# Optimization experiments

Measured on AMD Instinct MI355X. Metric: run time of the kernel, lower is better.

## Reference

```python
import jax, jax.numpy as jnp
import numpy as np

B, L, D = 2, 2048, 2048
H, KV, HD = 16, 4, 64  # query heads, kv heads, head_dim
EPS = 1e-6
ROPE_BASE = 10000.0


def setup_inputs() -> dict:
    key = jax.random.key(0)
    k0, k1, k2 = jax.random.split(key, 3)
    x = jax.random.normal(k0, (B, L, D), dtype=jnp.float32)
    W_qkv = jax.random.normal(k1, ((H + 2 * KV) * HD, D), dtype=jnp.float32) * 0.02
    W_out = jax.random.normal(k2, (D, H * HD), dtype=jnp.float32) * 0.02
    q_norm_w = jnp.ones((HD,), dtype=jnp.float32)
    k_norm_w = jnp.ones((HD,), dtype=jnp.float32)
    # causal additive mask (forward's optional `mask` arg)
    mask = jnp.triu(jnp.full((L, L), -1e9, dtype=jnp.float32), k=1)
    return {"x": x, "W_qkv": W_qkv, "W_out": W_out,
            "q_norm_w": q_norm_w, "k_norm_w": k_norm_w, "mask": mask}


def _rms_norm(x, w):
    # normalize over last (head) dim
    var = jnp.mean(x * x, axis=-1, keepdims=True)
    return x * jax.lax.rsqrt(var + EPS) * w


def _rope(x):
    # x: [B, nH, L, HD]; non-traditional (rotate-half) RoPE, offset=0
    half = HD // 2
    freqs = ROPE_BASE ** (-jnp.arange(0, HD, 2, dtype=jnp.float32) / HD)  # [half]
    theta = jnp.arange(L, dtype=jnp.float32)[:, None] * freqs[None, :]    # [L, half]
    cos, sin = jnp.cos(theta), jnp.sin(theta)
    x1, x2 = x[..., :half], x[..., half:]
    return jnp.concatenate([x1 * cos - x2 * sin, x1 * sin + x2 * cos], axis=-1)


def reference(x, W_qkv, W_out, q_norm_w, k_norm_w, mask):
    # fused QKV projection
    qkv = jnp.einsum("bld,ed->ble", x, W_qkv)                       # [B,L,(H+2KV)*HD]
    qkv = qkv.reshape(B, L, H + 2 * KV, HD).transpose(0, 2, 1, 3)   # [B,nH,L,HD]
    q, k, v = jnp.split(qkv, [H, H + KV], axis=1)
    # per-head QK RMSNorm + RoPE
    q = _rope(_rms_norm(q, q_norm_w))
    k = _rope(_rms_norm(k, k_norm_w))
    # GQA: repeat kv heads to match query heads
    rep = H // KV
    k = jnp.repeat(k, rep, axis=1)
    v = jnp.repeat(v, rep, axis=1)
    scale = HD ** -0.5
    scores = jnp.einsum("bhqd,bhkd->bhqk", q, k) * scale + mask      # [B,H,L,L]
    attn = jax.nn.softmax(scores, axis=-1)
    out = jnp.einsum("bhqk,bhkd->bhqd", attn, v)                     # [B,H,L,HD]
    out = out.transpose(0, 2, 1, 3).reshape(B, L, H * HD)
    return jnp.einsum("ble,de->bld", out, W_out)                     # [B,L,D]
```

## Files before the change

### kernel.cpp

```cpp
#include <hip/hip_runtime.h>
#include <hip/hip_bf16.h>


typedef __bf16 bf16;
typedef bf16 bf16x8 __attribute__((ext_vector_type(8)));
typedef bf16 bf16x4 __attribute__((ext_vector_type(4)));
typedef float f32x4 __attribute__((ext_vector_type(4)));

#define L_SEQ 2048
#define NQH 16
#define NKVH 4

__global__ __launch_bounds__(256) void cast_bf16(const float* __restrict__ in,
                                                 bf16* __restrict__ out, int n) {
  int i = (blockIdx.x * 256 + threadIdx.x) * 4;
  if (i < n) {
    float4 v = *(const float4*)&in[i];
    bf16x4 o;
    o[0] = (bf16)v.x; o[1] = (bf16)v.y; o[2] = (bf16)v.z; o[3] = (bf16)v.w;
    *(bf16x4*)&out[i] = o;
  }
}

__global__ __launch_bounds__(256)
void gemm_bt(const bf16* __restrict__ A, const bf16* __restrict__ B,
             float* __restrict__ C, int M, int N, int K) {
  __shared__ bf16 As[128 * 32];
  __shared__ bf16 Bs[128 * 32];
  const int tid = threadIdx.x;
  const int lane = tid & 63, w = tid >> 6;
  const int lq = lane & 15, g = lane >> 4;
  const int wr = w >> 1, wc = w & 1;
  const int bx = blockIdx.x, by = blockIdx.y;

  f32x4 acc[4][4] = {};

  const int nk = K >> 5;
  for (int kt = 0; kt < nk; ++kt) {
#pragma unroll
    for (int c = 0; c < 2; ++c) {
      int idx = c * 256 + tid;
      int row = idx >> 2;
      int ch = idx & 3;
      int pch = ch ^ ((row >> 1) & 3);
      bf16x8 va = *(const bf16x8*)&A[(size_t)(by * 128 + row) * K + kt * 32 + ch * 8];
      *(bf16x8*)&As[row * 32 + pch * 8] = va;
      bf16x8 vb = *(const bf16x8*)&B[(size_t)(bx * 128 + row) * K + kt * 32 + ch * 8];
      *(bf16x8*)&Bs[row * 32 + pch * 8] = vb;
    }
    __syncthreads();
    bf16x8 af[4], bfr[4];
#pragma unroll
    for (int i = 0; i < 4; ++i) {
      int ra = wr * 64 + i * 16 + lq;
      af[i] = *(const bf16x8*)&As[ra * 32 + (g ^ ((ra >> 1) & 3)) * 8];
      int rb = wc * 64 + i * 16 + lq;
      bfr[i] = *(const bf16x8*)&Bs[rb * 32 + (g ^ ((rb >> 1) & 3)) * 8];
    }
#pragma unroll
    for (int i = 0; i < 4; ++i)
#pragma unroll
      for (int j = 0; j < 4; ++j)
        acc[i][j] = __builtin_amdgcn_mfma_f32_16x16x32_bf16(af[i], bfr[j], acc[i][j], 0, 0, 0);
    __syncthreads();
  }
#pragma unroll
  for (int i = 0; i < 4; ++i)
#pragma unroll
    for (int j = 0; j < 4; ++j) {
      int row = by * 128 + wr * 64 + i * 16 + g * 4;
      int col = bx * 128 + wc * 64 + j * 16 + lq;
#pragma unroll
      for (int r = 0; r < 4; ++r) C[(size_t)(row + r) * N + col] = acc[i][j][r];
    }
}

__global__ __launch_bounds__(256)
void norm_rope(const float* __restrict__ qkv, const float* __restrict__ qw,
               const float* __restrict__ kw, bf16* __restrict__ Qb,
               bf16* __restrict__ Kb, bf16* __restrict__ Vb) {
  const int bl = blockIdx.x;
  const int b = bl >> 11, l = bl & (L_SEQ - 1);
  const int w = threadIdx.x >> 6, lane = threadIdx.x & 63;
  const int i = lane & 31;
  float freq = exp2f(-(float)i * 0.41524101186280154f);
  float theta = (float)l * freq;
  float sn, cs;
  sincosf(theta, &sn, &cs);
  float qwl = qw[lane], kwl = kw[lane];

  for (int h = w; h < 24; h += 4) {
    float v = qkv[(size_t)bl * 1536 + h * 64 + lane];
    if (h < 20) {
      float ss = v * v;
#pragma unroll
      for (int off = 32; off; off >>= 1) ss += __shfl_xor(ss, off);
      float rs = rsqrtf(ss * (1.f / 64.f) + 1e-6f);
      float wt = (h < 16) ? qwl : kwl;
      float y = v * rs * wt;
      float part = __shfl_xor(y, 32);
      float out = (lane < 32) ? (y * cs - part * sn) : (part * sn + y * cs);
      if (h < 16)
        Qb[((size_t)(b * NQH + h) * L_SEQ + l) * 64 + lane] = (bf16)(out * 0.125f);
      else
        Kb[((size_t)(b * NKVH + (h - 16)) * L_SEQ + l) * 64 + lane] = (bf16)out;
    } else {
      Vb[((size_t)(b * NKVH + (h - 20)) * L_SEQ + l) * 64 + lane] = (bf16)v;
    }
  }
}

__global__ __launch_bounds__(256)
void transpose_v(const bf16* __restrict__ Vb, bf16* __restrict__ Vt) {
  __shared__ bf16 T[64 * 66];
  const int bk = blockIdx.y;
  const int l0 = blockIdx.x * 64;
  const int t = threadIdx.x;
  const bf16* src = Vb + (size_t)bk * L_SEQ * 64;
#pragma unroll
  for (int c = 0; c < 2; ++c) {
    int idx = c * 256 + t;
    int row = idx >> 3, ch = idx & 7;
    bf16x8 v = *(const bf16x8*)&src[(size_t)(l0 + row) * 64 + ch * 8];
#pragma unroll
    for (int j = 0; j < 8; ++j) T[(ch * 8 + j) * 66 + row] = v[j];
  }
  __syncthreads();
  bf16* dst = Vt + (size_t)bk * 64 * L_SEQ;
#pragma unroll
  for (int c = 0; c < 2; ++c) {
    int idx = c * 256 + t;
    int d = idx >> 3, ch = idx & 7;
    bf16x8 v;
#pragma unroll
    for (int j = 0; j < 8; ++j) v[j] = T[d * 66 + ch * 8 + j];
    *(bf16x8*)&dst[(size_t)d * L_SEQ + l0 + ch * 8] = v;
  }
}

__global__ __launch_bounds__(256)
void attn(const bf16* __restrict__ Qb, const bf16* __restrict__ Kb,
          const bf16* __restrict__ Vt, bf16* __restrict__ Ao) {
  const int qblk = 31 - blockIdx.x;
  const int bh = blockIdx.y;
  const int b = bh >> 4, h = bh & 15, kv = h >> 2;
  const int tid = threadIdx.x;
  const int w = tid >> 6, lane = tid & 63;
  const int lq = lane & 15, g = lane >> 4;

  __shared__ bf16 Ks[64][64];
  __shared__ bf16 Vs[64][64];
  __shared__ bf16 Plds[4][16][72];

  const bf16* Qp = Qb + (size_t)(b * NQH + h) * L_SEQ * 64;
  const bf16* Kp = Kb + (size_t)(b * NKVH + kv) * L_SEQ * 64;
  const bf16* Vp = Vt + (size_t)(b * NKVH + kv) * 64 * L_SEQ;

  const int qr0 = qblk * 64 + w * 16;
  bf16x8 qf[2];
  qf[0] = *(const bf16x8*)&Qp[(qr0 + lq) * 64 + g * 8];
  qf[1] = *(const bf16x8*)&Qp[(qr0 + lq) * 64 + 32 + g * 8];

  const int sr0 = tid >> 3, sc = tid & 7;
  const int sr1 = sr0 + 32;
  const int swc0 = (sc ^ (sr0 & 7)) * 8;
  bf16x8 rk0, rk1, rv0, rv1;

  auto load_tile = [&](int k0) {
    rk0 = *(const bf16x8*)&Kp[(size_t)(k0 + sr0) * 64 + sc * 8];
    rk1 = *(const bf16x8*)&Kp[(size_t)(k0 + sr1) * 64 + sc * 8];
    rv0 = *(const bf16x8*)&Vp[(size_t)sr0 * L_SEQ + k0 + sc * 8];
    rv1 = *(const bf16x8*)&Vp[(size_t)sr1 * L_SEQ + k0 + sc * 8];
  };
  auto write_tile = [&]() {
    *(bf16x8*)&Ks[sr0][swc0] = rk0;
    *(bf16x8*)&Ks[sr1][swc0] = rk1;
    *(bf16x8*)&Vs[sr0][swc0] = rv0;
    *(bf16x8*)&Vs[sr1][swc0] = rv1;
  };

  f32x4 o[4] = {};
  float m = -1e30f, lsum = 0.f;
  const float L2E = 1.4426950408889634f;
  const int qg = qr0 + lq;

  const int nkt = qblk + 1;
  load_tile(0);
  write_tile();
  __syncthreads();

  for (int kt = 0; kt < nkt; ++kt) {
    const int k0 = kt * 64;
    const bool diag = (kt == nkt - 1);
    if (kt + 1 < nkt) load_tile(k0 + 64);

    f32x4 s[4] = {};
#pragma unroll
    for (int ks = 0; ks < 4; ++ks) {
      if (!diag || ks <= w) {
        const int row = ks * 16 + lq, sw = lq & 7;
        bf16x8 kf0 = *(const bf16x8*)&Ks[row][(g ^ sw) * 8];
        bf16x8 kf1 = *(const bf16x8*)&Ks[row][((g + 4) ^ sw) * 8];
        s[ks] = __builtin_amdgcn_mfma_f32_16x16x32_bf16(kf0, qf[0], s[ks], 0, 0, 0);
        s[ks] = __builtin_amdgcn_mfma_f32_16x16x32_bf16(kf1, qf[1], s[ks], 0, 0, 0);
      }
    }
    if (diag) {
#pragma unroll
      for (int ks = 0; ks < 4; ++ks)
#pragma unroll
        for (int r = 0; r < 4; ++r)
          if (k0 + ks * 16 + g * 4 + r > qg) s[ks][r] = -1e30f;
    }
    float tmax = -1e30f;
#pragma unroll
    for (int ks = 0; ks < 4; ++ks)
#pragma unroll
      for (int r = 0; r < 4; ++r) tmax = fmaxf(tmax, s[ks][r]);
    tmax = fmaxf(tmax, __shfl_xor(tmax, 16));
    tmax = fmaxf(tmax, __shfl_xor(tmax, 32));
    float mnew = fmaxf(m, tmax);
    float alpha = exp2f((m - mnew) * L2E);
    m = mnew;
    float rsum = 0.f;
#pragma unroll
    for (int ks = 0; ks < 4; ++ks) {
      bf16x4 p;
#pragma unroll
      for (int r = 0; r < 4; ++r) {
        float pv = exp2f((s[ks][r] - mnew) * L2E);
        rsum += pv;
        p[r] = (bf16)pv;
      }
      *(bf16x4*)&Plds[w][lq][ks * 16 + g * 4] = p;
    }
    rsum += __shfl_xor(rsum, 16);
    rsum += __shfl_xor(rsum, 32);
    lsum = lsum * alpha + rsum;

    float ar[4];
#pragma unroll
    for (int r = 0; r < 4; ++r) ar[r] = __shfl(alpha, (lane & 48) | (g * 4 + r));
#pragma unroll
    for (int dt = 0; dt < 4; ++dt)
#pragma unroll
      for (int r = 0; r < 4; ++r) o[dt][r] *= ar[r];

    bf16x8 pf0 = *(const bf16x8*)&Plds[w][lq][g * 8];
    bf16x8 pf1 = *(const bf16x8*)&Plds[w][lq][32 + g * 8];
#pragma unroll
    for (int dt = 0; dt < 4; ++dt) {
      const int row = dt * 16 + lq, sw = lq & 7;
      bf16x8 vf0 = *(const bf16x8*)&Vs[row][(g ^ sw) * 8];
      o[dt] = __builtin_amdgcn_mfma_f32_16x16x32_bf16(pf0, vf0, o[dt], 0, 0, 0);
      if (!diag || w >= 2) {
        bf16x8 vf1 = *(const bf16x8*)&Vs[row][((g + 4) ^ sw) * 8];
        o[dt] = __builtin_amdgcn_mfma_f32_16x16x32_bf16(pf1, vf1, o[dt], 0, 0, 0);
      }
    }

    if (kt + 1 < nkt) {
      __syncthreads();
      write_tile();
      __syncthreads();
    }
  }

  float linv = 1.f / lsum;
#pragma unroll
  for (int r = 0; r < 4; ++r) {
    float li = __shfl(linv, (lane & 48) | (g * 4 + r));
    int row = b * L_SEQ + qr0 + g * 4 + r;
#pragma unroll
    for (int dt = 0; dt < 4; ++dt)
      Ao[(size_t)row * 1024 + h * 64 + dt * 16 + lq] = (bf16)(o[dt][r] * li);
  }
}

extern "C" void kernel_launch(void* const* d_in, const int* in_sizes, int n_in,
                              void* d_out, int out_size, void* d_ws, size_t ws_size,
                              hipStream_t stream) {
  const float* x = (const float*)d_in[0];
  const float* Wqkv = (const float*)d_in[1];
  const float* Wout = (const float*)d_in[2];
  const float* qw = (const float*)d_in[3];
  const float* kw = (const float*)d_in[4];
  float* out = (float*)d_out;

  char* ws = (char*)d_ws;
  size_t off = 0;
  auto alloc = [&](size_t bytes) {
    void* p = ws + off;
    off = (off + bytes + 255) & ~(size_t)255;
    return p;
  };
  bf16* xb = (bf16*)alloc(8388608ull * 2);
  bf16* wqb = (bf16*)alloc(3145728ull * 2);
  bf16* wob = (bf16*)alloc(2097152ull * 2);
  float* qkv = (float*)alloc(4096ull * 1536 * 4);
  bf16* Qb = (bf16*)alloc(4194304ull * 2);
  bf16* Kb = (bf16*)alloc(1048576ull * 2);
  bf16* Vb = (bf16*)alloc(1048576ull * 2);
  bf16* Vt = (bf16*)alloc(1048576ull * 2);
  bf16* Ao = (bf16*)alloc(4194304ull * 2);

  cast_bf16<<<8192, 256, 0, stream>>>(x, xb, 8388608);
  cast_bf16<<<3072, 256, 0, stream>>>(Wqkv, wqb, 3145728);
  cast_bf16<<<2048, 256, 0, stream>>>(Wout, wob, 2097152);
  gemm_bt<<<dim3(12, 32), 256, 0, stream>>>(xb, wqb, qkv, 4096, 1536, 2048);
  norm_rope<<<4096, 256, 0, stream>>>(qkv, qw, kw, Qb, Kb, Vb);
  transpose_v<<<dim3(32, 8), 256, 0, stream>>>(Vb, Vt);
  attn<<<dim3(32, 32), 256, 0, stream>>>(Qb, Kb, Vt, Ao);
  gemm_bt<<<dim3(16, 32), 256, 0, stream>>>(Ao, wob, out, 4096, 2048, 1024);
}
```

Measured before the change: 303.5 us.

## Use async global-to-LDS loads in GEMM and pair causal query blocks in attention

```diff
diff --git a/kernel.cpp b/kernel.cpp
--- a/kernel.cpp
+++ b/kernel.cpp
@@ -10,6 +10,12 @@
 #define L_SEQ 2048
 #define NQH 16
 #define NKVH 4
+
+typedef __attribute__((address_space(3))) void lds_void;
+typedef const __attribute__((address_space(1))) void glb_void;
+__device__ __forceinline__ void async_ld16(const void* g, void* l) {
+  __builtin_amdgcn_global_load_lds((glb_void*)g, (lds_void*)l, 16, 0, 0);
+}
 
 __global__ __launch_bounds__(256) void cast_bf16(const float* __restrict__ in,
                                                  bf16* __restrict__ out, int n) {
@@ -33,20 +39,30 @@
   const int wr = w >> 1, wc = w & 1;
   const int bx = blockIdx.x, by = blockIdx.y;
 
+  const bf16* gA[2];
+  const bf16* gB[2];
+  bf16* ldsA[2];
+  bf16* ldsB[2];
+#pragma unroll
+  for (int c = 0; c < 2; ++c) {
+    int slot = c * 256 + tid;
+    int row = slot >> 2, ch = slot & 3;
+    int sch = ch ^ ((row >> 1) & 3);
+    gA[c] = &A[(size_t)(by * 128 + row) * K + sch * 8];
+    gB[c] = &B[(size_t)(bx * 128 + row) * K + sch * 8];
+    int wbase = (c * 256 + w * 64) * 8;
+    ldsA[c] = &As[wbase];
+    ldsB[c] = &Bs[wbase];
+  }
+
   f32x4 acc[4][4] = {};
 
   const int nk = K >> 5;
   for (int kt = 0; kt < nk; ++kt) {
 #pragma unroll
     for (int c = 0; c < 2; ++c) {
-      int idx = c * 256 + tid;
-      int row = idx >> 2;
-      int ch = idx & 3;
-      int pch = ch ^ ((row >> 1) & 3);
-      bf16x8 va = *(const bf16x8*)&A[(size_t)(by * 128 + row) * K + kt * 32 + ch * 8];
-      *(bf16x8*)&As[row * 32 + pch * 8] = va;
-      bf16x8 vb = *(const bf16x8*)&B[(size_t)(bx * 128 + row) * K + kt * 32 + ch * 8];
-      *(bf16x8*)&Bs[row * 32 + pch * 8] = vb;
+      async_ld16(gA[c] + kt * 32, ldsA[c]);
+      async_ld16(gB[c] + kt * 32, ldsB[c]);
     }
     __syncthreads();
     bf16x8 af[4], bfr[4];
@@ -141,7 +157,7 @@
 __global__ __launch_bounds__(256)
 void attn(const bf16* __restrict__ Qb, const bf16* __restrict__ Kb,
           const bf16* __restrict__ Vt, bf16* __restrict__ Ao) {
-  const int qblk = 31 - blockIdx.x;
+  const int pair = blockIdx.x;
   const int bh = blockIdx.y;
   const int b = bh >> 4, h = bh & 15, kv = h >> 2;
   const int tid = threadIdx.x;
@@ -155,11 +171,6 @@
   const bf16* Qp = Qb + (size_t)(b * NQH + h) * L_SEQ * 64;
   const bf16* Kp = Kb + (size_t)(b * NKVH + kv) * L_SEQ * 64;
   const bf16* Vp = Vt + (size_t)(b * NKVH + kv) * 64 * L_SEQ;
-
-  const int qr0 = qblk * 64 + w * 16;
-  bf16x8 qf[2];
-  qf[0] = *(const bf16x8*)&Qp[(qr0 + lq) * 64 + g * 8];
-  qf[1] = *(const bf16x8*)&Qp[(qr0 + lq) * 64 + 32 + g * 8];
 
   const int sr0 = tid >> 3, sc = tid & 7;
   const int sr1 = sr0 + 32;
@@ -179,101 +190,112 @@
     *(bf16x8*)&Vs[sr1][swc0] = rv1;
   };
 
-  f32x4 o[4] = {};
-  float m = -1e30f, lsum = 0.f;
   const float L2E = 1.4426950408889634f;
-  const int qg = qr0 + lq;
-
-  const int nkt = qblk + 1;
-  load_tile(0);
-  write_tile();
-  __syncthreads();
-
-  for (int kt = 0; kt < nkt; ++kt) {
-    const int k0 = kt * 64;
-    const bool diag = (kt == nkt - 1);
-    if (kt + 1 < nkt) load_tile(k0 + 64);
-
-    f32x4 s[4] = {};
-#pragma unroll
-    for (int ks = 0; ks < 4; ++ks) {
-      if (!diag || ks <= w) {
-        const int row = ks * 16 + lq, sw = lq & 7;
-        bf16x8 kf0 = *(const bf16x8*)&Ks[row][(g ^ sw) * 8];
-        bf16x8 kf1 = *(const bf16x8*)&Ks[row][((g + 4) ^ sw) * 8];
-        s[ks] = __builtin_amdgcn_mfma_f32_16x16x32_bf16(kf0, qf[0], s[ks], 0, 0, 0);
-        s[ks] = __builtin_amdgcn_mfma_f32_16x16x32_bf16(kf1, qf[1], s[ks], 0, 0, 0);
-      }
-    }
-    if (diag) {
+
+  for (int half = 0; half < 2; ++half) {
+    const int qblk = half ? (31 - pair) : pair;
+    const int qr0 = qblk * 64 + w * 16;
+    const int qg = qr0 + lq;
+
+    bf16x8 qf[2];
+    qf[0] = *(const bf16x8*)&Qp[(qr0 + lq) * 64 + g * 8];
+    qf[1] = *(const bf16x8*)&Qp[(qr0 + lq) * 64 + 32 + g * 8];
+
+    f32x4 o[4] = {};
+    float m = -1e30f, lsum = 0.f;
+
+    const int nkt = qblk + 1;
+    load_tile(0);
+    __syncthreads();
+    write_tile();
+    __syncthreads();
+
+    for (int kt = 0; kt < nkt; ++kt) {
+      const int k0 = kt * 64;
+      const bool diag = (kt == nkt - 1);
+      if (kt + 1 < nkt) load_tile(k0 + 64);
+
+      f32x4 s[4] = {};
+#pragma unroll
+      for (int ks = 0; ks < 4; ++ks) {
+        if (!diag || ks <= w) {
+          const int row = ks * 16 + lq, sw = lq & 7;
+          bf16x8 kf0 = *(const bf16x8*)&Ks[row][(g ^ sw) * 8];
+          bf16x8 kf1 = *(const bf16x8*)&Ks[row][((g + 4) ^ sw) * 8];
+          s[ks] = __builtin_amdgcn_mfma_f32_16x16x32_bf16(kf0, qf[0], s[ks], 0, 0, 0);
+          s[ks] = __builtin_amdgcn_mfma_f32_16x16x32_bf16(kf1, qf[1], s[ks], 0, 0, 0);
+        }
+      }
+      if (diag) {
+#pragma unroll
+        for (int ks = 0; ks < 4; ++ks)
+#pragma unroll
+          for (int r = 0; r < 4; ++r)
+            if (k0 + ks * 16 + g * 4 + r > qg) s[ks][r] = -1e30f;
+      }
+      float tmax = -1e30f;
 #pragma unroll
       for (int ks = 0; ks < 4; ++ks)
 #pragma unroll
-        for (int r = 0; r < 4; ++r)
-          if (k0 + ks * 16 + g * 4 + r > qg) s[ks][r] = -1e30f;
-    }
-    float tmax = -1e30f;
-#pragma unroll
-    for (int ks = 0; ks < 4; ++ks)
-#pragma unroll
-      for (int r = 0; r < 4; ++r) tmax = fmaxf(tmax, s[ks][r]);
-    tmax = fmaxf(tmax, __shfl_xor(tmax, 16));
-    tmax = fmaxf(tmax, __shfl_xor(tmax, 32));
-    float mnew = fmaxf(m, tmax);
-    float alpha = exp2f((m - mnew) * L2E);
-    m = mnew;
-    float rsum = 0.f;
-#pragma unroll
-    for (int ks = 0; ks < 4; ++ks) {
-      bf16x4 p;
-#pragma unroll
-      for (int r = 0; r < 4; ++r) {
-        float pv = exp2f((s[ks][r] - mnew) * L2E);
-        rsum += pv;
-        p[r] = (bf16)pv;
-      }
-      *(bf16x4*)&Plds[w][lq][ks * 16 + g * 4] = p;
-    }
-    rsum += __shfl_xor(rsum, 16);
-    rsum += __shfl_xor(rsum, 32);
-    lsum = lsum * alpha + rsum;
-
-    float ar[4];
-#pragma unroll
-    for (int r = 0; r < 4; ++r) ar[r] = __shfl(alpha, (lane & 48) | (g * 4 + r));
-#pragma unroll
-    for (int dt = 0; dt < 4; ++dt)
-#pragma unroll
-      for (int r = 0; r < 4; ++r) o[dt][r] *= ar[r];
-
-    bf16x8 pf0 = *(const bf16x8*)&Plds[w][lq][g * 8];
-    bf16x8 pf1 = *(const bf16x8*)&Plds[w][lq][32 + g * 8];
-#pragma unroll
-    for (int dt = 0; dt < 4; ++dt) {
-      const int row = dt * 16 + lq, sw = lq & 7;
-      bf16x8 vf0 = *(const bf16x8*)&Vs[row][(g ^ sw) * 8];
-      o[dt] = __builtin_amdgcn_mfma_f32_16x16x32_bf16(pf0, vf0, o[dt], 0, 0, 0);
-      if (!diag || w >= 2) {
-        bf16x8 vf1 = *(const bf16x8*)&Vs[row][((g + 4) ^ sw) * 8];
-        o[dt] = __builtin_amdgcn_mfma_f32_16x16x32_bf16(pf1, vf1, o[dt], 0, 0, 0);
-      }
-    }
-
-    if (kt + 1 < nkt) {
-      __syncthreads();
-      write_tile();
-      __syncthreads();
-    }
-  }
-
-  float linv = 1.f / lsum;
-#pragma unroll
-  for (int r = 0; r < 4; ++r) {
-    float li = __shfl(linv, (lane & 48) | (g * 4 + r));
-    int row = b * L_SEQ + qr0 + g * 4 + r;
-#pragma unroll
-    for (int dt = 0; dt < 4; ++dt)
-      Ao[(size_t)row * 1024 + h * 64 + dt * 16 + lq] = (bf16)(o[dt][r] * li);
+        for (int r = 0; r < 4; ++r) tmax = fmaxf(tmax, s[ks][r]);
+      tmax = fmaxf(tmax, __shfl_xor(tmax, 16));
+      tmax = fmaxf(tmax, __shfl_xor(tmax, 32));
+      float mnew = fmaxf(m, tmax);
+      float alpha = exp2f((m - mnew) * L2E);
+      m = mnew;
+      float rsum = 0.f;
+#pragma unroll
+      for (int ks = 0; ks < 4; ++ks) {
+        bf16x4 p;
+#pragma unroll
+        for (int r = 0; r < 4; ++r) {
+          float pv = exp2f((s[ks][r] - mnew) * L2E);
+          rsum += pv;
+          p[r] = (bf16)pv;
+        }
+        *(bf16x4*)&Plds[w][lq][ks * 16 + g * 4] = p;
+      }
+      rsum += __shfl_xor(rsum, 16);
+      rsum += __shfl_xor(rsum, 32);
+      lsum = lsum * alpha + rsum;
+
+      float ar[4];
+#pragma unroll
+      for (int r = 0; r < 4; ++r) ar[r] = __shfl(alpha, (lane & 48) | (g * 4 + r));
+#pragma unroll
+      for (int dt = 0; dt < 4; ++dt)
+#pragma unroll
+        for (int r = 0; r < 4; ++r) o[dt][r] *= ar[r];
+
+      bf16x8 pf0 = *(const bf16x8*)&Plds[w][lq][g * 8];
+      bf16x8 pf1 = *(const bf16x8*)&Plds[w][lq][32 + g * 8];
+#pragma unroll
+      for (int dt = 0; dt < 4; ++dt) {
+        const int row = dt * 16 + lq, sw = lq & 7;
+        bf16x8 vf0 = *(const bf16x8*)&Vs[row][(g ^ sw) * 8];
+        o[dt] = __builtin_amdgcn_mfma_f32_16x16x32_bf16(pf0, vf0, o[dt], 0, 0, 0);
+        if (!diag || w >= 2) {
+          bf16x8 vf1 = *(const bf16x8*)&Vs[row][((g + 4) ^ sw) * 8];
+          o[dt] = __builtin_amdgcn_mfma_f32_16x16x32_bf16(pf1, vf1, o[dt], 0, 0, 0);
+        }
+      }
+
+      if (kt + 1 < nkt) {
+        __syncthreads();
+        write_tile();
+        __syncthreads();
+      }
+    }
+
+    float linv = 1.f / lsum;
+#pragma unroll
+    for (int r = 0; r < 4; ++r) {
+      float li = __shfl(linv, (lane & 48) | (g * 4 + r));
+      int row = b * L_SEQ + qr0 + g * 4 + r;
+#pragma unroll
+      for (int dt = 0; dt < 4; ++dt)
+        Ao[(size_t)row * 1024 + h * 64 + dt * 16 + lq] = (bf16)(o[dt][r] * li);
+    }
   }
 }
 
@@ -310,6 +332,6 @@
   gemm_bt<<<dim3(12, 32), 256, 0, stream>>>(xb, wqb, qkv, 4096, 1536, 2048);
   norm_rope<<<4096, 256, 0, stream>>>(qkv, qw, kw, Qb, Kb, Vb);
   transpose_v<<<dim3(32, 8), 256, 0, stream>>>(Vb, Vt);
-  attn<<<dim3(32, 32), 256, 0, stream>>>(Qb, Kb, Vt, Ao);
+  attn<<<dim3(16, 32), 256, 0, stream>>>(Qb, Kb, Vt, Ao);
   gemm_bt<<<dim3(16, 32), 256, 0, stream>>>(Ao, wob, out, 4096, 2048, 1024);
 }
```

After: 282.5 us. -6.9%, faster.
